# Performance work log

Hardware: AMD Instinct MI355X
Metric: run time of the kernel (lower is better)

## Reference

```python
import jax, jax.numpy as jnp
import numpy as np

BB, F, K, D, H, HFF, L, M_PREV = 128, 8, 256, 256, 256, 512, 2, 2


def setup_inputs() -> dict:
    key = jax.random.key(0)
    ks = jax.random.split(key, 16)
    f32 = jnp.float32

    def lin(k, fan_in, shape):
        return (jax.random.normal(k, shape, dtype=f32) / np.sqrt(fan_in)).astype(f32)

    inp = {
        "x_BD": jax.random.normal(ks[0], (BB, D), dtype=f32),
        "xhat_BFD": jax.random.normal(ks[1], (BB, F, D), dtype=f32),
        "codes_MBF": jax.random.randint(ks[2], (M_PREV, BB, 1), 0, F * K, dtype=jnp.int64),
        "codebook": jax.random.normal(ks[3], (K, D), dtype=f32) / np.sqrt(D),
        "W_in": lin(ks[4], D, (D, H)),
        "b_in": jnp.zeros((H,), f32),
        # concat projection over cat([h, xhat], -1): (H + D) -> H
        "W_cat": lin(ks[5], H + D, (H + D, H)),
        "b_cat": jnp.zeros((H,), f32),
        "W1": lin(ks[6], H, (L, H, HFF)),
        "b1": jnp.zeros((L, HFF), f32),
        "W2": lin(ks[7], HFF, (L, HFF, H)),
        "b2": jnp.zeros((L, H), f32),
        "W_out": lin(ks[8], H, (H, D)),
        "b_out": jnp.zeros((D,), f32),
    }
    return inp


def reference(x_BD, xhat_BFD, codes_MBF, codebook, W_in, b_in, W_cat, b_cat,
              W1, b1, W2, b2, W_out, b_out):
    Bb, Fb, Dd = xhat_BFD.shape
    Kk = codebook.shape[0]

    # in_proj applied to the (shared) codebook once: [K, H]
    h0 = codebook @ W_in + b_in

    # concat(h, xhat) as a linear over the concatenation, split to avoid
    # materializing a [Bb,F,K,H+D] tensor.
    Wc, Wx = W_cat[:H], W_cat[H:]
    h = (h0 @ Wc)[None, None] + (xhat_BFD @ Wx)[:, :, None] + b_cat  # [Bb,F,K,H]

    # residual MLP blocks: h <- h + W2 relu(W1 h)
    for l in range(L):
        h = h + jax.nn.relu(h @ W1[l] + b1[l]) @ W2[l] + b2[l]

    # out_proj + residual codeword (res_codeword_coeff = 1.0) + xhat offset
    cw = h @ W_out + b_out + codebook[None, None]        # [Bb,F,K,D]
    cw = cw + xhat_BFD[:, :, None]                        # reconstructed candidates

    cflat = cw.reshape(Bb, Fb * Kk, Dd)                   # [Bb, F*K, D]

    dists = (jnp.sum(x_BD * x_BD, -1, keepdims=True)
             - 2.0 * jnp.einsum('bd,bkd->bk', x_BD, cflat)
             + jnp.sum(cflat * cflat, -1))                # [Bb, F*K]

    idx = jnp.argmin(dists, axis=-1)                      # [Bb]
    xhat_next_BFD = jnp.take_along_axis(cflat, idx[:, None, None], axis=1)  # [Bb,1,D]

    codes_new = jnp.concatenate(
        [codes_MBF, idx[None, :, None].astype(codes_MBF.dtype)], axis=0)
    return xhat_next_BFD, codes_new
```

## Files before the change

kernel.cpp:

```cpp
#include <hip/hip_runtime.h>
#include <hip/hip_bf16.h>

#define B_   128
#define F_   8
#define K_   256
#define D_   256
#define H_   256
#define HFF_ 512
#define RT   64

typedef _Float16 half8  __attribute__((ext_vector_type(8)));
typedef _Float16 half4v __attribute__((ext_vector_type(4)));
typedef float floatx4   __attribute__((ext_vector_type(4)));

#define MFMAH(a,b,c) __builtin_amdgcn_mfma_f32_16x16x32_f16(a,b,c,0,0,0)

#define HA_S  260
#define HMA_S 132

__global__ void k_prep(const float* __restrict__ cb, const float* __restrict__ Win,
                       const float* __restrict__ bin, const float* __restrict__ Wcat,
                       const float* __restrict__ bcat, const float* __restrict__ xhat,
                       const float* __restrict__ W1, const float* __restrict__ W2,
                       const float* __restrict__ Wout,
                       float* __restrict__ u, float* __restrict__ v,
                       _Float16* __restrict__ w1f, _Float16* __restrict__ w2f,
                       _Float16* __restrict__ wof) {
  const int blk = blockIdx.x, t = threadIdx.x;
  if (blk < K_) {
    __shared__ float row[D_];
    __shared__ float h0row[H_];
    row[t] = cb[blk * D_ + t];
    __syncthreads();
    float a0 = 0.f, a1 = 0.f, a2 = 0.f, a3 = 0.f;
    #pragma unroll 4
    for (int i = 0; i < 64; ++i) {
      a0 = fmaf(row[i      ], Win[(i      ) * H_ + t], a0);
      a1 = fmaf(row[i +  64], Win[(i +  64) * H_ + t], a1);
      a2 = fmaf(row[i + 128], Win[(i + 128) * H_ + t], a2);
      a3 = fmaf(row[i + 192], Win[(i + 192) * H_ + t], a3);
    }
    h0row[t] = bin[t] + ((a0 + a1) + (a2 + a3));
    __syncthreads();
    float c0 = 0.f, c1 = 0.f, c2 = 0.f, c3 = 0.f;
    #pragma unroll 4
    for (int i = 0; i < 64; ++i) {
      c0 = fmaf(h0row[i      ], Wcat[(i      ) * H_ + t], c0);
      c1 = fmaf(h0row[i +  64], Wcat[(i +  64) * H_ + t], c1);
      c2 = fmaf(h0row[i + 128], Wcat[(i + 128) * H_ + t], c2);
      c3 = fmaf(h0row[i + 192], Wcat[(i + 192) * H_ + t], c3);
    }
    u[blk * H_ + t] = (c0 + c1) + (c2 + c3);
  } else if (blk < K_ + B_ * F_) {
    __shared__ float row2[D_];
    const int bf = blk - K_;
    row2[t] = xhat[bf * D_ + t];
    __syncthreads();
    float a0 = 0.f, a1 = 0.f, a2 = 0.f, a3 = 0.f;
    #pragma unroll 4
    for (int i = 0; i < 64; ++i) {
      a0 = fmaf(row2[i      ], Wcat[(H_ + i      ) * H_ + t], a0);
      a1 = fmaf(row2[i +  64], Wcat[(H_ + i +  64) * H_ + t], a1);
      a2 = fmaf(row2[i + 128], Wcat[(H_ + i + 128) * H_ + t], a2);
      a3 = fmaf(row2[i + 192], Wcat[(H_ + i + 192) * H_ + t], a3);
    }
    v[bf * H_ + t] = bcat[t] + ((a0 + a1) + (a2 + a3));
  } else {
    const int e = (blk - (K_ + B_ * F_)) * 256 + t;
    const float* src; _Float16* dst; int N, NT, le;
    if (e < 262144) {
      const int layer = e >> 17; le = e & 131071;
      src = W1 + layer * (H_ * HFF_); dst = w1f + layer * (H_ * HFF_);
      N = HFF_; NT = 32;
    } else if (e < 524288) {
      const int e2 = e - 262144;
      const int layer = e2 >> 17; le = e2 & 131071;
      src = W2 + layer * (HFF_ * H_); dst = w2f + layer * (HFF_ * H_);
      N = H_; NT = 16;
    } else {
      le = e - 524288; src = Wout; dst = wof; N = D_; NT = 16;
    }
    const int jj = le & 7, lane = (le >> 3) & 63, r = le >> 9;
    const int ntile = r % NT, kstep = r / NT;
    const int row = kstep * 32 + (lane >> 4) * 8 + jj;
    const int colc = ntile * 16 + (lane & 15);
    dst[le] = (_Float16)src[row * N + colc];
  }
}

__global__ __launch_bounds__(256, 3) void k_main(
    const float* __restrict__ u, const float* __restrict__ v,
    const _Float16* __restrict__ w1f, const float* __restrict__ b1,
    const _Float16* __restrict__ w2f, const float* __restrict__ b2,
    const _Float16* __restrict__ woutf, const float* __restrict__ bout,
    const float* __restrict__ cb, const float* __restrict__ xhat,
    const float* __restrict__ x, float* __restrict__ dists) {
  __shared__ _Float16 hA[64][HA_S];
  __shared__ _Float16 hmA[64][HMA_S];
  __shared__ float x_s[D_], xh_s[D_];
  __shared__ float dist_s[4][64];

  const int t = threadIdx.x;
  const int blk = blockIdx.x;
  const int bf = blk >> 2, k0 = (blk & 3) << 6;
  const int b = bf >> 3, f = bf & 7;
  const int wave = t >> 6, lane = t & 63;
  const int col = lane & 15, quad = lane >> 4;
  const int lane8 = lane * 8;

  x_s[t]  = x[b * D_ + t];
  xh_s[t] = xhat[bf * D_ + t];

  {
    const int r = t >> 2, c0 = (t & 3) * 64;
    const float* up = u + (k0 + r) * H_ + c0;
    const float* vp = v + bf * H_ + c0;
    #pragma unroll
    for (int j = 0; j < 64; j += 8) {
      float4 uA = *(const float4*)(up + j);
      float4 vA = *(const float4*)(vp + j);
      float4 uB = *(const float4*)(up + j + 4);
      float4 vB = *(const float4*)(vp + j + 4);
      half8 hv8;
      hv8[0] = (_Float16)(uA.x + vA.x); hv8[1] = (_Float16)(uA.y + vA.y);
      hv8[2] = (_Float16)(uA.z + vA.z); hv8[3] = (_Float16)(uA.w + vA.w);
      hv8[4] = (_Float16)(uB.x + vB.x); hv8[5] = (_Float16)(uB.y + vB.y);
      hv8[6] = (_Float16)(uB.z + vB.z); hv8[7] = (_Float16)(uB.w + vB.w);
      *(half8*)&hA[r][c0 + j] = hv8;
    }
  }
  __syncthreads();

  const floatx4 zero4 = {0.f, 0.f, 0.f, 0.f};

  #pragma unroll 1
  for (int l = 0; l < 2; ++l) {
    const _Float16* w1_l = w1f + l * (H_ * HFF_);
    const _Float16* w2_l = w2f + l * (HFF_ * H_);
    const float* b1l = b1 + l * HFF_;
    const float* b2l = b2 + l * H_;

    floatx4 acc2[4][4];
    #pragma unroll
    for (int mt = 0; mt < 4; ++mt)
      #pragma unroll
      for (int nt = 0; nt < 4; ++nt) acc2[mt][nt] = zero4;

    #pragma unroll 1
    for (int ch = 0; ch < 4; ++ch) {
      floatx4 acc1[2][4];
      #pragma unroll
      for (int mt = 0; mt < 2; ++mt)
        #pragma unroll
        for (int nt = 0; nt < 4; ++nt) acc1[mt][nt] = zero4;

      const _Float16* w1_b = w1_l + (ch * 8 + wave * 2) * 512 + lane8;

      __builtin_amdgcn_s_setprio(1);
      #pragma unroll 4
      for (int ks = 0; ks < 8; ++ks) {
        half8 b0 = *(const half8*)&hA[col][ks * 32 + quad * 8];
        half8 b1v = *(const half8*)&hA[16 + col][ks * 32 + quad * 8];
        half8 b2v = *(const half8*)&hA[32 + col][ks * 32 + quad * 8];
        half8 b3v = *(const half8*)&hA[48 + col][ks * 32 + quad * 8];
        const int ko = ks * 32 * 512;
        #pragma unroll
        for (int mt = 0; mt < 2; ++mt) {
          half8 aw = *(const half8*)(w1_b + ko + mt * 512);
          acc1[mt][0] = MFMAH(aw, b0, acc1[mt][0]);
          acc1[mt][1] = MFMAH(aw, b1v, acc1[mt][1]);
          acc1[mt][2] = MFMAH(aw, b2v, acc1[mt][2]);
          acc1[mt][3] = MFMAH(aw, b3v, acc1[mt][3]);
        }
      }
      __builtin_amdgcn_s_setprio(0);
      #pragma unroll
      for (int mt = 0; mt < 2; ++mt) {
        const int floc = (wave * 2 + mt) * 16 + quad * 4;
        float4 bb = *(const float4*)&b1l[ch * 128 + floc];
        #pragma unroll
        for (int nt = 0; nt < 4; ++nt) {
          const int row = nt * 16 + col;
          half4v nh;
          #pragma unroll
          for (int p = 0; p < 4; ++p)
            nh[p] = (_Float16)fmaxf(acc1[mt][nt][p] + ((const float*)&bb)[p], 0.f);
          *(half4v*)&hmA[row][floc] = nh;
        }
      }
      __syncthreads();

      const _Float16* w2_b = w2_l + (ch * 64 + wave * 4) * 512 + lane8;
      __builtin_amdgcn_s_setprio(1);
      #pragma unroll 2
      for (int ks = 0; ks < 4; ++ks) {
        half8 b0 = *(const half8*)&hmA[col][ks * 32 + quad * 8];
        half8 b1v = *(const half8*)&hmA[16 + col][ks * 32 + quad * 8];
        half8 b2v = *(const half8*)&hmA[32 + col][ks * 32 + quad * 8];
        half8 b3v = *(const half8*)&hmA[48 + col][ks * 32 + quad * 8];
        const int ko = ks * 16 * 512;
        #pragma unroll
        for (int mt = 0; mt < 4; ++mt) {
          half8 aw = *(const half8*)(w2_b + ko + mt * 512);
          acc2[mt][0] = MFMAH(aw, b0, acc2[mt][0]);
          acc2[mt][1] = MFMAH(aw, b1v, acc2[mt][1]);
          acc2[mt][2] = MFMAH(aw, b2v, acc2[mt][2]);
          acc2[mt][3] = MFMAH(aw, b3v, acc2[mt][3]);
        }
      }
      __builtin_amdgcn_s_setprio(0);
      __syncthreads();
    }

    #pragma unroll
    for (int mt = 0; mt < 4; ++mt) {
      const int feat0 = (wave * 4 + mt) * 16 + quad * 4;
      float4 bb = *(const float4*)&b2l[feat0];
      #pragma unroll
      for (int nt = 0; nt < 4; ++nt) {
        const int row = nt * 16 + col;
        half4v oh = *(half4v*)&hA[row][feat0];
        half4v nh;
        #pragma unroll
        for (int p = 0; p < 4; ++p)
          nh[p] = (_Float16)((float)oh[p] + acc2[mt][nt][p] + ((const float*)&bb)[p]);
        *(half4v*)&hA[row][feat0] = nh;
      }
    }
    __syncthreads();
  }

  floatx4 acc3[4][4];
  #pragma unroll
  for (int mt = 0; mt < 4; ++mt)
    #pragma unroll
    for (int nt = 0; nt < 4; ++nt) acc3[mt][nt] = zero4;

  const _Float16* wo_b = woutf + (wave * 4) * 512 + lane8;
  __builtin_amdgcn_s_setprio(1);
  #pragma unroll 2
  for (int ks = 0; ks < 8; ++ks) {
    half8 b0 = *(const half8*)&hA[col][ks * 32 + quad * 8];
    half8 b1v = *(const half8*)&hA[16 + col][ks * 32 + quad * 8];
    half8 b2v = *(const half8*)&hA[32 + col][ks * 32 + quad * 8];
    half8 b3v = *(const half8*)&hA[48 + col][ks * 32 + quad * 8];
    const int ko = ks * 16 * 512;
    #pragma unroll
    for (int mt = 0; mt < 4; ++mt) {
      half8 aw = *(const half8*)(wo_b + ko + mt * 512);
      acc3[mt][0] = MFMAH(aw, b0, acc3[mt][0]);
      acc3[mt][1] = MFMAH(aw, b1v, acc3[mt][1]);
      acc3[mt][2] = MFMAH(aw, b2v, acc3[mt][2]);
      acc3[mt][3] = MFMAH(aw, b3v, acc3[mt][3]);
    }
  }
  __builtin_amdgcn_s_setprio(0);

  float s[4] = {0.f, 0.f, 0.f, 0.f};
  #pragma unroll
  for (int mt = 0; mt < 4; ++mt) {
    const int d0 = (wave * 4 + mt) * 16 + quad * 4;
    float4 bo = *(const float4*)&bout[d0];
    float4 xv = *(const float4*)&x_s[d0];
    float4 xh4 = *(const float4*)&xh_s[d0];
    #pragma unroll
    for (int nt = 0; nt < 4; ++nt) {
      float4 cbv = *(const float4*)&cb[(k0 + nt * 16 + col) * D_ + d0];
      #pragma unroll
      for (int p = 0; p < 4; ++p) {
        float base = ((const float*)&bo)[p] + ((const float*)&xh4)[p];
        float xx = ((const float*)&xv)[p];
        float cw = acc3[mt][nt][p] + base + ((const float*)&cbv)[p];
        s[nt] += cw * (cw - 2.f * xx);
      }
    }
  }
  #pragma unroll
  for (int nt = 0; nt < 4; ++nt) {
    s[nt] += __shfl_xor(s[nt], 16, 64);
    s[nt] += __shfl_xor(s[nt], 32, 64);
  }
  if (quad == 0) {
    #pragma unroll
    for (int nt = 0; nt < 4; ++nt)
      dist_s[wave][nt * 16 + col] = s[nt];
  }
  __syncthreads();
  if (t < 64) {
    float d = dist_s[0][t] + dist_s[1][t] + dist_s[2][t] + dist_s[3][t];
    dists[b * (F_ * K_) + f * K_ + k0 + t] = d;
  }
}

__global__ void k_top8(const float* __restrict__ dists, int* __restrict__ topi) {
  __shared__ float ds[F_ * K_];
  __shared__ float bv[512];
  __shared__ int bi_s[512];
  const int b = blockIdx.x, t = threadIdx.x;
  for (int j = t; j < F_ * K_; j += 512) ds[j] = dists[b * (F_ * K_) + j];
  __syncthreads();
  for (int pass = 0; pass < 8; ++pass) {
    float best = 3.4e38f; int bi = 0;
    for (int j = t; j < F_ * K_; j += 512) {
      const float dv = ds[j];
      if (dv < best) { best = dv; bi = j; }
    }
    bv[t] = best; bi_s[t] = bi;
    __syncthreads();
    for (int s = 256; s > 0; s >>= 1) {
      if (t < s) {
        const float ov = bv[t + s]; const int oi = bi_s[t + s];
        if (ov < bv[t] || (ov == bv[t] && oi < bi_s[t])) { bv[t] = ov; bi_s[t] = oi; }
      }
      __syncthreads();
    }
    if (t == 0) { topi[b * 8 + pass] = bi_s[0]; ds[bi_s[0]] = 3.4e38f; }
    __syncthreads();
  }
}

#define NCL 2
__global__ __launch_bounds__(512) void k_resfin(
    const float* __restrict__ u, const float* __restrict__ v,
    const float* __restrict__ W1, const float* __restrict__ b1,
    const float* __restrict__ W2, const float* __restrict__ b2,
    const float* __restrict__ Wout, const float* __restrict__ bout,
    const float* __restrict__ cb, const float* __restrict__ xhat,
    const float* __restrict__ x, const int* __restrict__ topi,
    float* __restrict__ resc2, int* __restrict__ iwin2,
    float* __restrict__ cwhalf) {
  __shared__ float hs4[4][H_ + 4];
  __shared__ float hms4[4][HFF_ + 4];
  __shared__ float cw4[4][H_ + 4];
  __shared__ float redw[8][NCL];
  __shared__ int   sel_sh;

  const int blk = blockIdx.x;
  const int b = blk >> 1, half = blk & 1;
  const int t = threadIdx.x;
  const int g = t >> 8, tloc = t & 255;
  const int wave = t >> 6, lane = t & 63;
  const int cbase = half * 4;

  int kc[NCL], bfc[NCL];
  #pragma unroll
  for (int cl = 0; cl < NCL; ++cl) {
    const int ix = topi[b * 8 + cbase + g * 2 + cl];
    kc[cl] = ix & 255;
    bfc[cl] = b * F_ + (ix >> 8);
  }

  #pragma unroll
  for (int cl = 0; cl < NCL; ++cl)
    hs4[g * 2 + cl][tloc] = u[kc[cl] * H_ + tloc] + v[bfc[cl] * H_ + tloc];
  __syncthreads();

  #pragma unroll 1
  for (int l = 0; l < 2; ++l) {
    const float* W1l = W1 + l * (H_ * HFF_);
    const float* W2l = W2 + l * (HFF_ * H_);

    float a0[NCL], a1[NCL];
    {
      const float bb0 = b1[l * HFF_ + tloc], bb1 = b1[l * HFF_ + 256 + tloc];
      #pragma unroll
      for (int cl = 0; cl < NCL; ++cl) { a0[cl] = bb0; a1[cl] = bb1; }
    }
    #pragma unroll 2
    for (int i = 0; i < H_; i += 4) {
      float4 hv[NCL];
      #pragma unroll
      for (int cl = 0; cl < NCL; ++cl) hv[cl] = *(const float4*)&hs4[g * 2 + cl][i];
      #pragma unroll
      for (int q = 0; q < 4; ++q) {
        const float w0 = W1l[(i + q) * HFF_ + tloc];
        const float w1 = W1l[(i + q) * HFF_ + 256 + tloc];
        #pragma unroll
        for (int cl = 0; cl < NCL; ++cl) {
          const float h = ((const float*)&hv[cl])[q];
          a0[cl] = fmaf(h, w0, a0[cl]);
          a1[cl] = fmaf(h, w1, a1[cl]);
        }
      }
    }
    #pragma unroll
    for (int cl = 0; cl < NCL; ++cl) {
      hms4[g * 2 + cl][tloc] = fmaxf(a0[cl], 0.f);
      hms4[g * 2 + cl][tloc + 256] = fmaxf(a1[cl], 0.f);
    }
    __syncthreads();

    float hn[NCL];
    {
      const float bb2 = b2[l * H_ + tloc];
      #pragma unroll
      for (int cl = 0; cl < NCL; ++cl) hn[cl] = hs4[g * 2 + cl][tloc] + bb2;
    }
    #pragma unroll 2
    for (int jj = 0; jj < HFF_; jj += 4) {
      float4 hv[NCL];
      #pragma unroll
      for (int cl = 0; cl < NCL; ++cl) hv[cl] = *(const float4*)&hms4[g * 2 + cl][jj];
      #pragma unroll
      for (int q = 0; q < 4; ++q) {
        const float w = W2l[(jj + q) * H_ + tloc];
        #pragma unroll
        for (int cl = 0; cl < NCL; ++cl)
          hn[cl] = fmaf(((const float*)&hv[cl])[q], w, hn[cl]);
      }
    }
    __syncthreads();
    #pragma unroll
    for (int cl = 0; cl < NCL; ++cl) hs4[g * 2 + cl][tloc] = hn[cl];
    __syncthreads();
  }

  float cw[NCL];
  {
    const float bo = bout[tloc];
    #pragma unroll
    for (int cl = 0; cl < NCL; ++cl)
      cw[cl] = bo + cb[kc[cl] * D_ + tloc] + xhat[bfc[cl] * D_ + tloc];
  }
  #pragma unroll 2
  for (int i = 0; i < H_; i += 4) {
    float4 hv[NCL];
    #pragma unroll
    for (int cl = 0; cl < NCL; ++cl) hv[cl] = *(const float4*)&hs4[g * 2 + cl][i];
    #pragma unroll
    for (int q = 0; q < 4; ++q) {
      const float w = Wout[(i + q) * D_ + tloc];
      #pragma unroll
      for (int cl = 0; cl < NCL; ++cl)
        cw[cl] = fmaf(((const float*)&hv[cl])[q], w, cw[cl]);
    }
  }

  const float xx = x[b * D_ + tloc];
  #pragma unroll
  for (int cl = 0; cl < NCL; ++cl) {
    cw4[g * 2 + cl][tloc] = cw[cl];
    float vsum = cw[cl] * (cw[cl] - 2.f * xx);
    vsum += __shfl_xor(vsum, 1, 64);
    vsum += __shfl_xor(vsum, 2, 64);
    vsum += __shfl_xor(vsum, 4, 64);
    vsum += __shfl_xor(vsum, 8, 64);
    vsum += __shfl_xor(vsum, 16, 64);
    vsum += __shfl_xor(vsum, 32, 64);
    if (lane == 0) redw[wave][cl] = vsum;
  }
  __syncthreads();
  if (t == 0) {
    float bd = 3.4e38f; int bidx = 1 << 30; int bc = 0;
    #pragma unroll
    for (int c = 0; c < 4; ++c) {
      const int gg = c >> 1, cl = c & 1;
      const float d = redw[gg * 4 + 0][cl] + redw[gg * 4 + 1][cl] +
                      redw[gg * 4 + 2][cl] + redw[gg * 4 + 3][cl];
      const int ix = topi[b * 8 + cbase + c];
      if (d < bd || (d == bd && ix < bidx)) { bd = d; bidx = ix; bc = c; }
    }
    resc2[blk] = bd;
    iwin2[blk] = bidx;
    sel_sh = bc;
  }
  __syncthreads();
  if (t < 256) cwhalf[blk * 256 + t] = cw4[sel_sh][t];
}

__global__ void k_finw(const float* __restrict__ resc2, const int* __restrict__ iwin2,
                       const float* __restrict__ cwhalf, const int* __restrict__ codes,
                       float* __restrict__ out) {
  const int b = blockIdx.x, t = threadIdx.x;
  const float d0 = resc2[b * 2], d1 = resc2[b * 2 + 1];
  const int i0 = iwin2[b * 2], i1 = iwin2[b * 2 + 1];
  const int sel = (d1 < d0 || (d1 == d0 && i1 < i0)) ? 1 : 0;
  out[b * D_ + t] = cwhalf[(b * 2 + sel) * 256 + t];
  if (t < 2)
    out[B_ * D_ + t * B_ + b] = (float)codes[t * B_ + b];
  else if (t == 2)
    out[B_ * D_ + 2 * B_ + b] = (float)(sel ? i1 : i0);
}

extern "C" void kernel_launch(void* const* d_in, const int* in_sizes, int n_in,
                              void* d_out, int out_size, void* d_ws, size_t ws_size,
                              hipStream_t stream) {
  const float* x    = (const float*)d_in[0];
  const float* xhat = (const float*)d_in[1];
  const int*   codes= (const int*)d_in[2];
  const float* cb   = (const float*)d_in[3];
  const float* Win  = (const float*)d_in[4];
  const float* bin  = (const float*)d_in[5];
  const float* Wcat = (const float*)d_in[6];
  const float* bcat = (const float*)d_in[7];
  const float* W1   = (const float*)d_in[8];
  const float* b1   = (const float*)d_in[9];
  const float* W2   = (const float*)d_in[10];
  const float* b2   = (const float*)d_in[11];
  const float* Wout = (const float*)d_in[12];
  const float* bout = (const float*)d_in[13];
  float* out = (float*)d_out;

  float* u     = (float*)d_ws;
  float* v     = u + K_ * H_;
  float* dists = v + B_ * F_ * H_;
  float* resc  = dists + B_ * F_ * K_;
  int*   topi  = (int*)(resc + 1024);
  int*   pad   = topi + 1024;
  _Float16* w1f  = (_Float16*)(pad + 128);
  _Float16* w2f  = w1f + 2 * H_ * HFF_;
  _Float16* wof  = w2f + 2 * HFF_ * H_;

  float* resc2  = resc;
  int*   iwin2  = (int*)(resc + 256);
  float* cwhalf = dists;

  k_prep<<<K_ + B_ * F_ + 2304, 256, 0, stream>>>(cb, Win, bin, Wcat, bcat, xhat,
                                                  W1, W2, Wout, u, v, w1f, w2f, wof);

  k_main<<<B_ * F_ * (K_ / RT), 256, 0, stream>>>(u, v, w1f, b1, w2f, b2,
                                                  wof, bout, cb, xhat, x, dists);
  k_top8<<<B_, 512, 0, stream>>>(dists, topi);
  k_resfin<<<2 * B_, 512, 0, stream>>>(u, v, W1, b1, W2, b2, Wout, bout, cb, xhat,
                                       x, topi, resc2, iwin2, cwhalf);
  k_finw<<<B_, 256, 0, stream>>>(resc2, iwin2, cwhalf, codes, out);
}
```

Measured before the change: 521.9 us.

## Precompute first-layer W1 projections of separable u and v terms

Before the first MLP layer, h is the sum of a per-codeword term u and a per-(b,f) term v, so h@W1 splits into u@W1 plus v@W1. A new kernel precomputes both projections once (K + B*F rows instead of B*F*K), and k_main's layer-0 first GEMM becomes an fp16 add plus ReLU of the two precomputed rows. This removes about a quarter of the main kernel's MFMA work. In exchange it adds a scalar fp32 prep kernel and extra global reads, and it sums in fp16, which changes rounding before the ReLU.

```diff
diff --git a/kernel.cpp b/kernel.cpp
--- a/kernel.cpp
+++ b/kernel.cpp
@@ -88,13 +88,49 @@
   }
 }
 
+__global__ void k_prep2(const float* __restrict__ u, const float* __restrict__ v,
+                        const float* __restrict__ W1, const float* __restrict__ b1,
+                        _Float16* __restrict__ pre_u, _Float16* __restrict__ pre_v) {
+  __shared__ float row[H_];
+  const int blk = blockIdx.x, t = threadIdx.x;
+  const bool is_u = (blk < K_);
+  const int idx = is_u ? blk : (blk - K_);
+  const float* src = is_u ? (u + idx * H_) : (v + idx * H_);
+  row[t] = src[t];
+  __syncthreads();
+  float a0 = 0.f, a1 = 0.f, a2 = 0.f, a3 = 0.f;
+  float c0 = 0.f, c1 = 0.f, c2 = 0.f, c3 = 0.f;
+  #pragma unroll 4
+  for (int i = 0; i < 64; ++i) {
+    const float r0 = row[i], r1 = row[i + 64], r2 = row[i + 128], r3 = row[i + 192];
+    a0 = fmaf(r0, W1[(i      ) * HFF_ + t], a0);
+    a1 = fmaf(r1, W1[(i +  64) * HFF_ + t], a1);
+    a2 = fmaf(r2, W1[(i + 128) * HFF_ + t], a2);
+    a3 = fmaf(r3, W1[(i + 192) * HFF_ + t], a3);
+    c0 = fmaf(r0, W1[(i      ) * HFF_ + 256 + t], c0);
+    c1 = fmaf(r1, W1[(i +  64) * HFF_ + 256 + t], c1);
+    c2 = fmaf(r2, W1[(i + 128) * HFF_ + 256 + t], c2);
+    c3 = fmaf(r3, W1[(i + 192) * HFF_ + 256 + t], c3);
+  }
+  const float s0 = (a0 + a1) + (a2 + a3);
+  const float s1 = (c0 + c1) + (c2 + c3);
+  if (is_u) {
+    pre_u[idx * HFF_ + t] = (_Float16)s0;
+    pre_u[idx * HFF_ + 256 + t] = (_Float16)s1;
+  } else {
+    pre_v[idx * HFF_ + t] = (_Float16)(s0 + b1[t]);
+    pre_v[idx * HFF_ + 256 + t] = (_Float16)(s1 + b1[256 + t]);
+  }
+}
+
 __global__ __launch_bounds__(256, 3) void k_main(
     const float* __restrict__ u, const float* __restrict__ v,
     const _Float16* __restrict__ w1f, const float* __restrict__ b1,
     const _Float16* __restrict__ w2f, const float* __restrict__ b2,
     const _Float16* __restrict__ woutf, const float* __restrict__ bout,
     const float* __restrict__ cb, const float* __restrict__ xhat,
-    const float* __restrict__ x, float* __restrict__ dists) {
+    const float* __restrict__ x, const _Float16* __restrict__ pre_u,
+    const _Float16* __restrict__ pre_v, float* __restrict__ dists) {
   __shared__ _Float16 hA[64][HA_S];
   __shared__ _Float16 hmA[64][HMA_S];
   __shared__ float x_s[D_], xh_s[D_];
@@ -148,44 +184,62 @@
 
     #pragma unroll 1
     for (int ch = 0; ch < 4; ++ch) {
-      floatx4 acc1[2][4];
-      #pragma unroll
-      for (int mt = 0; mt < 2; ++mt)
-        #pragma unroll
-        for (int nt = 0; nt < 4; ++nt) acc1[mt][nt] = zero4;
-
-      const _Float16* w1_b = w1_l + (ch * 8 + wave * 2) * 512 + lane8;
-
-      __builtin_amdgcn_s_setprio(1);
-      #pragma unroll 4
-      for (int ks = 0; ks < 8; ++ks) {
-        half8 b0 = *(const half8*)&hA[col][ks * 32 + quad * 8];
-        half8 b1v = *(const half8*)&hA[16 + col][ks * 32 + quad * 8];
-        half8 b2v = *(const half8*)&hA[32 + col][ks * 32 + quad * 8];
-        half8 b3v = *(const half8*)&hA[48 + col][ks * 32 + quad * 8];
-        const int ko = ks * 32 * 512;
+      if (l == 0) {
+        const int r = t >> 2, c0 = (t & 3) * 32;
+        const _Float16* pup = pre_u + (k0 + r) * HFF_ + ch * 128 + c0;
+        const _Float16* pvp = pre_v + bf * HFF_ + ch * 128 + c0;
+        #pragma unroll
+        for (int j = 0; j < 32; j += 8) {
+          half8 pu = *(const half8*)(pup + j);
+          half8 pv = *(const half8*)(pvp + j);
+          half8 hm;
+          #pragma unroll
+          for (int p = 0; p < 8; ++p) {
+            const _Float16 s = pu[p] + pv[p];
+            hm[p] = s > (_Float16)0.f ? s : (_Float16)0.f;
+          }
+          *(half8*)&hmA[r][c0 + j] = hm;
+        }
+      } else {
+        floatx4 acc1[2][4];
+        #pragma unroll
+        for (int mt = 0; mt < 2; ++mt)
+          #pragma unroll
+          for (int nt = 0; nt < 4; ++nt) acc1[mt][nt] = zero4;
+
+        const _Float16* w1_b = w1_l + (ch * 8 + wave * 2) * 512 + lane8;
+
+        __builtin_amdgcn_s_setprio(1);
+        #pragma unroll 4
+        for (int ks = 0; ks < 8; ++ks) {
+          half8 b0 = *(const half8*)&hA[col][ks * 32 + quad * 8];
+          half8 b1v = *(const half8*)&hA[16 + col][ks * 32 + quad * 8];
+          half8 b2v = *(const half8*)&hA[32 + col][ks * 32 + quad * 8];
+          half8 b3v = *(const half8*)&hA[48 + col][ks * 32 + quad * 8];
+          const int ko = ks * 32 * 512;
+          #pragma unroll
+          for (int mt = 0; mt < 2; ++mt) {
+            half8 aw = *(const half8*)(w1_b + ko + mt * 512);
+            acc1[mt][0] = MFMAH(aw, b0, acc1[mt][0]);
+            acc1[mt][1] = MFMAH(aw, b1v, acc1[mt][1]);
+            acc1[mt][2] = MFMAH(aw, b2v, acc1[mt][2]);
+            acc1[mt][3] = MFMAH(aw, b3v, acc1[mt][3]);
+          }
+        }
+        __builtin_amdgcn_s_setprio(0);
         #pragma unroll
         for (int mt = 0; mt < 2; ++mt) {
-          half8 aw = *(const half8*)(w1_b + ko + mt * 512);
-          acc1[mt][0] = MFMAH(aw, b0, acc1[mt][0]);
-          acc1[mt][1] = MFMAH(aw, b1v, acc1[mt][1]);
-          acc1[mt][2] = MFMAH(aw, b2v, acc1[mt][2]);
-          acc1[mt][3] = MFMAH(aw, b3v, acc1[mt][3]);
-        }
-      }
-      __builtin_amdgcn_s_setprio(0);
-      #pragma unroll
-      for (int mt = 0; mt < 2; ++mt) {
-        const int floc = (wave * 2 + mt) * 16 + quad * 4;
-        float4 bb = *(const float4*)&b1l[ch * 128 + floc];
-        #pragma unroll
-        for (int nt = 0; nt < 4; ++nt) {
-          const int row = nt * 16 + col;
-          half4v nh;
+          const int floc = (wave * 2 + mt) * 16 + quad * 4;
+          float4 bb = *(const float4*)&b1l[ch * 128 + floc];
           #pragma unroll
-          for (int p = 0; p < 4; ++p)
-            nh[p] = (_Float16)fmaxf(acc1[mt][nt][p] + ((const float*)&bb)[p], 0.f);
-          *(half4v*)&hmA[row][floc] = nh;
+          for (int nt = 0; nt < 4; ++nt) {
+            const int row = nt * 16 + col;
+            half4v nh;
+            #pragma unroll
+            for (int p = 0; p < 4; ++p)
+              nh[p] = (_Float16)fmaxf(acc1[mt][nt][p] + ((const float*)&bb)[p], 0.f);
+            *(half4v*)&hmA[row][floc] = nh;
+          }
         }
       }
       __syncthreads();
@@ -510,6 +564,8 @@
   _Float16* w1f  = (_Float16*)(pad + 128);
   _Float16* w2f  = w1f + 2 * H_ * HFF_;
   _Float16* wof  = w2f + 2 * HFF_ * H_;
+  _Float16* pre_u = wof + H_ * D_;
+  _Float16* pre_v = pre_u + K_ * HFF_;
 
   float* resc2  = resc;
   int*   iwin2  = (int*)(resc + 256);
@@ -517,9 +573,11 @@
 
   k_prep<<<K_ + B_ * F_ + 2304, 256, 0, stream>>>(cb, Win, bin, Wcat, bcat, xhat,
                                                   W1, W2, Wout, u, v, w1f, w2f, wof);
+  k_prep2<<<K_ + B_ * F_, 256, 0, stream>>>(u, v, W1, b1, pre_u, pre_v);
 
   k_main<<<B_ * F_ * (K_ / RT), 256, 0, stream>>>(u, v, w1f, b1, w2f, b2,
-                                                  wof, bout, cb, xhat, x, dists);
+                                                  wof, bout, cb, xhat, x,
+                                                  pre_u, pre_v, dists);
   k_top8<<<B_, 512, 0, stream>>>(dists, topi);
   k_resfin<<<2 * B_, 512, 0, stream>>>(u, v, W1, b1, W2, b2, Wout, bout, cb, xhat,
                                        x, topi, resc2, iwin2, cwhalf);
```

Result: faster. 502.7 us (-3.7%).
